# Optimization experiments

Hardware: AMD Instinct MI355X
Metric: run time of the kernel (lower is better)

## Reference

```python
import math
import jax, jax.numpy as jnp
import numpy as np

ETA = 0.3      # eta_threshold
EPS = 1e-08

B, S, C_IN, D_MODEL = 16, 2048, 64, 512


def setup_inputs() -> dict:
    key = jax.random.key(0)
    k1, k2, k3, k4 = jax.random.split(key, 4)
    x = jax.random.normal(k1, (B, S, C_IN), dtype=jnp.float32)
    # Conv1d(c_in, d_model, kernel=3, bias=False), kaiming fan_in
    fan_in = C_IN * 3
    conv_w = jax.random.normal(k2, (D_MODEL, C_IN, 3), dtype=jnp.float32) * (2.0 / fan_in) ** 0.5
    # Linear(1, d_model)
    tc_w = jax.random.normal(k3, (D_MODEL, 1), dtype=jnp.float32) * 0.5
    tc_b = jax.random.normal(k4, (D_MODEL,), dtype=jnp.float32) * 0.1
    return {"x": x, "conv_w": conv_w, "tc_w": tc_w, "tc_b": tc_b}


def compute_tc_vector(x):
    # x: (B, S, N_s). L1 norm over channels (beta_norm == 1).
    norms = jnp.sum(jnp.abs(x), axis=-1)            # (B, S)
    thresh = (1.0 - ETA) * (norms + EPS)            # condition: norms[s] < thresh[t]
    s = norms.shape[1]
    idx = jnp.arange(s)
    causal = idx[None, :] < idx[:, None]            # (T, S): s < t
    lt = norms[:, None, :] < thresh[:, :, None]     # (B, T, S)
    mask = lt & causal[None]
    # smallest tau = largest s with condition true; tau = t - s
    s_max = jnp.max(jnp.where(mask, idx[None, None, :], -1), axis=-1)  # (B, T)
    tc = jnp.where(s_max >= 0, idx[None, :] - s_max, 0)
    return tc.astype(jnp.float32)


def positional_embedding(seq_len, d_model):
    position = jnp.arange(seq_len, dtype=jnp.float32)[:, None]
    div_term = jnp.exp(jnp.arange(0, d_model, 2, dtype=jnp.float32) * (-math.log(10000.0) / d_model))
    ang = position * div_term                        # (S, D/2)
    pe = jnp.zeros((seq_len, d_model), dtype=jnp.float32)
    pe = pe.at[:, 0::2].set(jnp.sin(ang)).at[:, 1::2].set(jnp.cos(ang))
    return pe


def reference(x, conv_w, tc_w, tc_b):
    b, s, c = x.shape
    d = conv_w.shape[0]
    # Tc embedding: (B,S) -> Linear(1, D)
    tc = compute_tc_vector(x)                        # (B, S)
    tc_embed = tc[..., None] * tc_w[:, 0][None, None, :] + tc_b  # (B, S, D)
    # Token embedding: circular conv1d, k=3, pad 1 each side, no bias
    xc = jnp.transpose(x, (0, 2, 1))                 # (B, C, S)
    xp = jnp.concatenate([xc[..., -1:], xc, xc[..., :1]], axis=-1)
    conv = jax.lax.conv_general_dilated(xp, conv_w, window_strides=(1,), padding='VALID', dimension_numbers=('NCH', 'OIH', 'NCH'))
    val = jnp.transpose(conv, (0, 2, 1))             # (B, S, D)
    pe = positional_embedding(s, d)                  # (S, D)
    # dropout is identity in eval mode
    return val + pe[None] + tc_embed
```

## Files before the change

### kernel.cpp

```cpp
#include <hip/hip_runtime.h>
#include <hip/hip_bf16.h>

typedef __attribute__((ext_vector_type(8))) short bfrag;
typedef __attribute__((ext_vector_type(4))) float f32x4;

typedef __attribute__((address_space(1))) const void GV;
typedef __attribute__((address_space(3))) void LV;

static __device__ __forceinline__ float b2f(short s) {
    unsigned u = ((unsigned)(unsigned short)s) << 16;
    float f;
    __builtin_memcpy(&f, &u, 4);
    return f;
}

__global__ void k_prep(const float* __restrict__ x,
                       const float* __restrict__ w,
                       const float* __restrict__ tcb,
                       float* __restrict__ norms,
                       __hip_bfloat16* __restrict__ xb,
                       __hip_bfloat16* __restrict__ wt,
                       __hip_bfloat16* __restrict__ pe2b) {
    int blk = blockIdx.x;
    if (blk < 2048) {
        int i = blk * 256 + threadIdx.x;
        f32x4 v = *(const f32x4*)&x[i * 4];
        __hip_bfloat16 h[4];
        h[0] = __float2bfloat16(v.x);
        h[1] = __float2bfloat16(v.y);
        h[2] = __float2bfloat16(v.z);
        h[3] = __float2bfloat16(v.w);
        *(short4*)&xb[i * 4] = *(const short4*)h;
        float a = fabsf(v.x) + fabsf(v.y) + fabsf(v.z) + fabsf(v.w);
        a += __shfl_xor(a, 1);
        a += __shfl_xor(a, 2);
        a += __shfl_xor(a, 4);
        a += __shfl_xor(a, 8);
        if ((threadIdx.x & 15) == 0) norms[i >> 4] = a;
    } else if (blk < 2432) {
        int i = (blk - 2048) * 256 + threadIdx.x;
        int d = i / 192, kk = i - d * 192;
        int c = kk & 63, k = kk >> 6;
        wt[i] = __float2bfloat16(w[d * 192 + c * 3 + k]);
    } else {
        int j = (blk - 2432) * 256 + threadIdx.x;
        int s = j >> 7, q = j & 127;
        f32x4 tb = *(const f32x4*)&tcb[q * 4];
        float dv0 = expf((float)(4 * q)     * (-9.210340371976184f / 512.0f));
        float dv1 = expf((float)(4 * q + 2) * (-9.210340371976184f / 512.0f));
        float s0v, c0v, s1v, c1v;
        sincosf((float)s * dv0, &s0v, &c0v);
        sincosf((float)s * dv1, &s1v, &c1v);
        __hip_bfloat16 h[4];
        h[0] = __float2bfloat16(s0v + tb.x);
        h[1] = __float2bfloat16(c0v + tb.y);
        h[2] = __float2bfloat16(s1v + tb.z);
        h[3] = __float2bfloat16(c1v + tb.w);
        *(short4*)&pe2b[s * 512 + q * 4] = *(const short4*)h;
    }
}

__global__ void k_tc(const float* __restrict__ norms, float* __restrict__ tc) {
    int gid = blockIdx.x * 256 + threadIdx.x;
    int wave = gid >> 6;
    int lane = threadIdx.x & 63;
    int b = wave >> 11, t = wave & 2047;
    const float* nb = norms + (b << 11);
    float thresh = 0.7f * (nb[t] + 1e-8f);
    int res = 0;
    for (int W = (t - 1) >> 8; W >= 0; --W) {
        int sBase = W * 256 + 4 * lane;
        f32x4 v = *(const f32x4*)&nb[sBase];
        int best = -1;
        if (sBase + 0 < t && v.x < thresh) best = sBase + 0;
        if (sBase + 1 < t && v.y < thresh) best = sBase + 1;
        if (sBase + 2 < t && v.z < thresh) best = sBase + 2;
        if (sBase + 3 < t && v.w < thresh) best = sBase + 3;
        unsigned long long m = __ballot(best >= 0);
        if (m) {
            int L = 63 - __clzll(m);
            int smax = __shfl(best, L);
            res = t - smax;
            break;
        }
    }
    if (lane == 0) tc[wave] = (float)res;
}

__launch_bounds__(256, 3)
__global__ void k_gemm(const __hip_bfloat16* __restrict__ xb,
                       const __hip_bfloat16* __restrict__ wt,
                       const __hip_bfloat16* __restrict__ pe2b,
                       const float* __restrict__ tc,
                       const float* __restrict__ tcw,
                       float* __restrict__ out) {
    __shared__ alignas(16) __hip_bfloat16 Bs[130 * 64];
    __shared__ alignas(16) __hip_bfloat16 Ps[128 * 128];
    __shared__ alignas(16) float Ts[128];

    const int bid = blockIdx.x;
    const int xcd = bid & 7, u = bid >> 3;
    const int st = (xcd << 1) | (u & 1);
    const int bb = (u >> 1) & 15;
    const int d0 = (u >> 5) << 7;
    const int s0 = st << 7;
    const int tid = threadIdx.x;
    const int lane = tid & 63;
    const int wd = tid >> 6;
    const int lhi = lane >> 4, ll = lane & 15;

#pragma unroll
    for (int i = 0; i < 5; ++i) {
        int q = tid + i * 256;
        if (q < 1040) {
            int row = q >> 3, uu = q & 7;
            int us = uu ^ (row & 7);
            int sg = (s0 - 1 + row) & 2047;
            const __hip_bfloat16* src =
                xb + (size_t)((bb << 11) + sg) * 64 + us * 8;
            __builtin_amdgcn_global_load_lds((GV*)src, (LV*)(Bs + q * 8), 16, 0, 0);
        }
    }

    const __hip_bfloat16* wbase =
        wt + (size_t)(d0 + wd * 32 + ll) * 192 + lhi * 8;
    bfrag af[3][2][2];
#pragma unroll
    for (int k = 0; k < 3; ++k)
#pragma unroll
        for (int kc = 0; kc < 2; ++kc)
#pragma unroll
            for (int m = 0; m < 2; ++m)
                af[k][kc][m] = *(const bfrag*)(wbase + m * 16 * 192 +
                                               k * 64 + kc * 32);

    __syncthreads();

#pragma unroll
    for (int i = 0; i < 8; ++i) {
        int q = tid + i * 256;
        int sl = q >> 4, c = q & 15;
        int cs = c ^ (sl & 7);
        const __hip_bfloat16* src = pe2b + (size_t)(s0 + sl) * 512 + d0 + cs * 8;
        __builtin_amdgcn_global_load_lds((GV*)src, (LV*)(Ps + q * 8), 16, 0, 0);
    }
    if (tid < 32) {
        const float* src = tc + (bb << 11) + s0 + tid * 4;
        __builtin_amdgcn_global_load_lds((GV*)src, (LV*)(Ts + tid * 4), 16, 0, 0);
    }
    f32x4 tw[2];
#pragma unroll
    for (int m = 0; m < 2; ++m)
        tw[m] = *(const f32x4*)&tcw[d0 + wd * 32 + m * 16 + lhi * 4];

    f32x4 acc[2][8] = {};
#pragma unroll
    for (int k = 0; k < 3; ++k) {
#pragma unroll
        for (int kc = 0; kc < 2; ++kc) {
            const int colB = kc * 64 + lhi * 16;
            bfrag bf[8];
#pragma unroll
            for (int n = 0; n < 8; ++n) {
                int rl = n * 16 + ll + k;
                bf[n] = *(const bfrag*)((const char*)Bs + rl * 128 +
                                        (colB ^ ((rl & 7) << 4)));
            }
#pragma unroll
            for (int m = 0; m < 2; ++m)
#pragma unroll
                for (int n = 0; n < 8; ++n)
                    acc[m][n] = __builtin_amdgcn_mfma_f32_16x16x32_bf16(
                        af[k][kc][m], bf[n], acc[m][n], 0, 0, 0);
        }
    }

    __syncthreads();

#pragma unroll
    for (int n = 0; n < 8; ++n) {
        const int sl = n * 16 + ll;
        const int sCol = s0 + sl;
        const float tcv = Ts[sl];
        const size_t orow = ((size_t)(bb << 11) + sCol) * 512;
#pragma unroll
        for (int m = 0; m < 2; ++m) {
            const int dloc = wd * 32 + m * 16 + lhi * 4;
            const int pbyte = sl * 256 + ((((dloc >> 3) ^ (sl & 7)) << 4) |
                                          ((dloc << 1) & 15));
            const short4 pv = *(const short4*)((const char*)Ps + pbyte);
            f32x4 r = acc[m][n];
            r.x += b2f(pv.x) + tcv * tw[m].x;
            r.y += b2f(pv.y) + tcv * tw[m].y;
            r.z += b2f(pv.z) + tcv * tw[m].z;
            r.w += b2f(pv.w) + tcv * tw[m].w;
            *(f32x4*)&out[orow + d0 + dloc] = r;
        }
    }
}

extern "C" void kernel_launch(void* const* d_in, const int* in_sizes, int n_in,
                              void* d_out, int out_size, void* d_ws, size_t ws_size,
                              hipStream_t stream) {
    const float* x   = (const float*)d_in[0];
    const float* cw  = (const float*)d_in[1];
    const float* tcw = (const float*)d_in[2];
    const float* tcb = (const float*)d_in[3];
    float* out = (float*)d_out;

    char* ws = (char*)d_ws;
    __hip_bfloat16* xb   = (__hip_bfloat16*)(ws);
    __hip_bfloat16* wt   = (__hip_bfloat16*)(ws + 4194304);
    __hip_bfloat16* pe2b = (__hip_bfloat16*)(ws + 4390912);
    float* norms         = (float*)(ws + 6488064);
    float* tc            = (float*)(ws + 6619136);

    hipLaunchKernelGGL(k_prep, dim3(3456), dim3(256), 0, stream,
                       x, cw, tcb, norms, xb, wt, pe2b);
    hipLaunchKernelGGL(k_tc,   dim3(8192), dim3(256), 0, stream, norms, tc);
    hipLaunchKernelGGL(k_gemm, dim3(1024), dim3(256), 0, stream,
                       xb, wt, pe2b, tc, tcw, out);
}
```

Baseline: 40.25 us.

## Split positional tile into halves aliasing LDS to raise gemm occupancy

Cuts the gemm kernel's LDS footprint by loading the positional/bias tile in two 64-row halves. The second half reuses the input tile's LDS region once the MFMA loop has finished with it. Launch bounds go from 3 to 4 blocks per CU so more blocks can be resident. The cost is an extra barrier and loading the second half after compute, which exposes its latency in the epilogue. The tighter bound may also cause register spills.

```diff
diff --git a/kernel.cpp b/kernel.cpp
--- a/kernel.cpp
+++ b/kernel.cpp
@@ -87,16 +87,18 @@
     if (lane == 0) tc[wave] = (float)res;
 }
 
-__launch_bounds__(256, 3)
+__launch_bounds__(256, 4)
 __global__ void k_gemm(const __hip_bfloat16* __restrict__ xb,
                        const __hip_bfloat16* __restrict__ wt,
                        const __hip_bfloat16* __restrict__ pe2b,
                        const float* __restrict__ tc,
                        const float* __restrict__ tcw,
                        float* __restrict__ out) {
-    __shared__ alignas(16) __hip_bfloat16 Bs[130 * 64];
-    __shared__ alignas(16) __hip_bfloat16 Ps[128 * 128];
-    __shared__ alignas(16) float Ts[128];
+    __shared__ alignas(16) char Smem[33536];
+    __hip_bfloat16* Bs = (__hip_bfloat16*)Smem;
+    float* Ts          = (float*)(Smem + 16640);
+    char* Ps1          = Smem + 17152;
+    char* Ps2          = Smem;
 
     const int bid = blockIdx.x;
     const int xcd = bid & 7, u = bid >> 3;
@@ -121,6 +123,10 @@
             __builtin_amdgcn_global_load_lds((GV*)src, (LV*)(Bs + q * 8), 16, 0, 0);
         }
     }
+    if (tid < 32) {
+        const float* src = tc + (bb << 11) + s0 + tid * 4;
+        __builtin_amdgcn_global_load_lds((GV*)src, (LV*)(Ts + tid * 4), 16, 0, 0);
+    }
 
     const __hip_bfloat16* wbase =
         wt + (size_t)(d0 + wd * 32 + ll) * 192 + lhi * 8;
@@ -133,25 +139,21 @@
             for (int m = 0; m < 2; ++m)
                 af[k][kc][m] = *(const bfrag*)(wbase + m * 16 * 192 +
                                                k * 64 + kc * 32);
+    f32x4 tw[2];
+#pragma unroll
+    for (int m = 0; m < 2; ++m)
+        tw[m] = *(const f32x4*)&tcw[d0 + wd * 32 + m * 16 + lhi * 4];
 
     __syncthreads();
 
 #pragma unroll
-    for (int i = 0; i < 8; ++i) {
+    for (int i = 0; i < 4; ++i) {
         int q = tid + i * 256;
         int sl = q >> 4, c = q & 15;
         int cs = c ^ (sl & 7);
         const __hip_bfloat16* src = pe2b + (size_t)(s0 + sl) * 512 + d0 + cs * 8;
-        __builtin_amdgcn_global_load_lds((GV*)src, (LV*)(Ps + q * 8), 16, 0, 0);
-    }
-    if (tid < 32) {
-        const float* src = tc + (bb << 11) + s0 + tid * 4;
-        __builtin_amdgcn_global_load_lds((GV*)src, (LV*)(Ts + tid * 4), 16, 0, 0);
-    }
-    f32x4 tw[2];
-#pragma unroll
-    for (int m = 0; m < 2; ++m)
-        tw[m] = *(const f32x4*)&tcw[d0 + wd * 32 + m * 16 + lhi * 4];
+        __builtin_amdgcn_global_load_lds((GV*)src, (LV*)(Ps1 + q * 16), 16, 0, 0);
+    }
 
     f32x4 acc[2][8] = {};
 #pragma unroll
@@ -178,7 +180,17 @@
     __syncthreads();
 
 #pragma unroll
-    for (int n = 0; n < 8; ++n) {
+    for (int i = 0; i < 4; ++i) {
+        int q = tid + i * 256;
+        int r = q >> 4, c = q & 15;
+        int cs = c ^ (r & 7);
+        const __hip_bfloat16* src =
+            pe2b + (size_t)(s0 + 64 + r) * 512 + d0 + cs * 8;
+        __builtin_amdgcn_global_load_lds((GV*)src, (LV*)(Ps2 + q * 16), 16, 0, 0);
+    }
+
+#pragma unroll
+    for (int n = 0; n < 4; ++n) {
         const int sl = n * 16 + ll;
         const int sCol = s0 + sl;
         const float tcv = Ts[sl];
@@ -188,7 +200,31 @@
             const int dloc = wd * 32 + m * 16 + lhi * 4;
             const int pbyte = sl * 256 + ((((dloc >> 3) ^ (sl & 7)) << 4) |
                                           ((dloc << 1) & 15));
-            const short4 pv = *(const short4*)((const char*)Ps + pbyte);
+            const short4 pv = *(const short4*)(Ps1 + pbyte);
+            f32x4 r = acc[m][n];
+            r.x += b2f(pv.x) + tcv * tw[m].x;
+            r.y += b2f(pv.y) + tcv * tw[m].y;
+            r.z += b2f(pv.z) + tcv * tw[m].z;
+            r.w += b2f(pv.w) + tcv * tw[m].w;
+            *(f32x4*)&out[orow + d0 + dloc] = r;
+        }
+    }
+
+    __syncthreads();
+
+#pragma unroll
+    for (int n = 4; n < 8; ++n) {
+        const int sl = n * 16 + ll;
+        const int r2 = sl - 64;
+        const int sCol = s0 + sl;
+        const float tcv = Ts[sl];
+        const size_t orow = ((size_t)(bb << 11) + sCol) * 512;
+#pragma unroll
+        for (int m = 0; m < 2; ++m) {
+            const int dloc = wd * 32 + m * 16 + lhi * 4;
+            const int pbyte = r2 * 256 + ((((dloc >> 3) ^ (r2 & 7)) << 4) |
+                                          ((dloc << 1) & 15));
+            const short4 pv = *(const short4*)(Ps2 + pbyte);
             f32x4 r = acc[m][n];
             r.x += b2f(pv.x) + tcv * tw[m].x;
             r.y += b2f(pv.y) + tcv * tw[m].y;
```

Result: slower. 52.61 us (+30.7%).

## Process four batches per GEMM block to reuse weights and positional tile

Applied to the files above, without the earlier changes.

Each GEMM block now covers four batch elements for the same sequence/d_model tile. It loads all four x tiles into a larger shared buffer, and loads the weight fragments, PE tile and tc weights once, then loops over the batches. The grid shrinks from 1024 to 256 blocks and occupancy drops to one block per CU because of about 100KB of LDS. The aim is to cut redundant weight and PE loads, at the cost of less parallelism and latency hiding for a store-bound kernel.

```diff
diff --git a/kernel.cpp b/kernel.cpp
--- a/kernel.cpp
+++ b/kernel.cpp
@@ -87,22 +87,22 @@
     if (lane == 0) tc[wave] = (float)res;
 }
 
-__launch_bounds__(256, 3)
+__launch_bounds__(256, 1)
 __global__ void k_gemm(const __hip_bfloat16* __restrict__ xb,
                        const __hip_bfloat16* __restrict__ wt,
                        const __hip_bfloat16* __restrict__ pe2b,
                        const float* __restrict__ tc,
                        const float* __restrict__ tcw,
                        float* __restrict__ out) {
-    __shared__ alignas(16) __hip_bfloat16 Bs[130 * 64];
-    __shared__ alignas(16) __hip_bfloat16 Ps[128 * 128];
-    __shared__ alignas(16) float Ts[128];
+    __shared__ alignas(16) char Smem[101376];
+    char* Ps1 = Smem + 66560;
+    float* Ts = (float*)(Smem + 99328);
 
     const int bid = blockIdx.x;
-    const int xcd = bid & 7, u = bid >> 3;
-    const int st = (xcd << 1) | (u & 1);
-    const int bb = (u >> 1) & 15;
-    const int d0 = (u >> 5) << 7;
+    const int xcd = bid & 7, v = bid >> 3;
+    const int st = (xcd << 1) | (v & 1);
+    const int bbg = (v >> 1) & 3;
+    const int d0 = (v >> 3) << 7;
     const int s0 = st << 7;
     const int tid = threadIdx.x;
     const int lane = tid & 63;
@@ -110,91 +110,99 @@
     const int lhi = lane >> 4, ll = lane & 15;
 
 #pragma unroll
-    for (int i = 0; i < 5; ++i) {
-        int q = tid + i * 256;
-        if (q < 1040) {
-            int row = q >> 3, uu = q & 7;
-            int us = uu ^ (row & 7);
-            int sg = (s0 - 1 + row) & 2047;
-            const __hip_bfloat16* src =
-                xb + (size_t)((bb << 11) + sg) * 64 + us * 8;
-            __builtin_amdgcn_global_load_lds((GV*)src, (LV*)(Bs + q * 8), 16, 0, 0);
-        }
-    }
-
-    const __hip_bfloat16* wbase =
-        wt + (size_t)(d0 + wd * 32 + ll) * 192 + lhi * 8;
-    bfrag af[3][2][2];
-#pragma unroll
-    for (int k = 0; k < 3; ++k)
-#pragma unroll
-        for (int kc = 0; kc < 2; ++kc)
-#pragma unroll
-            for (int m = 0; m < 2; ++m)
-                af[k][kc][m] = *(const bfrag*)(wbase + m * 16 * 192 +
-                                               k * 64 + kc * 32);
-
-    __syncthreads();
-
+    for (int bi = 0; bi < 4; ++bi) {
+        const size_t xrow = (size_t)((bbg * 4 + bi) << 11);
+        char* Bsb = Smem + bi * 16640;
+#pragma unroll
+        for (int i = 0; i < 5; ++i) {
+            int q = tid + i * 256;
+            if (q < 1040) {
+                int row = q >> 3, uu = q & 7;
+                int us = uu ^ (row & 7);
+                int sg = (s0 - 1 + row) & 2047;
+                const __hip_bfloat16* src = xb + (xrow + sg) * 64 + us * 8;
+                __builtin_amdgcn_global_load_lds((GV*)src, (LV*)(Bsb + q * 16),
+                                                 16, 0, 0);
+            }
+        }
+    }
 #pragma unroll
     for (int i = 0; i < 8; ++i) {
         int q = tid + i * 256;
         int sl = q >> 4, c = q & 15;
         int cs = c ^ (sl & 7);
         const __hip_bfloat16* src = pe2b + (size_t)(s0 + sl) * 512 + d0 + cs * 8;
-        __builtin_amdgcn_global_load_lds((GV*)src, (LV*)(Ps + q * 8), 16, 0, 0);
-    }
-    if (tid < 32) {
-        const float* src = tc + (bb << 11) + s0 + tid * 4;
-        __builtin_amdgcn_global_load_lds((GV*)src, (LV*)(Ts + tid * 4), 16, 0, 0);
-    }
+        __builtin_amdgcn_global_load_lds((GV*)src, (LV*)(Ps1 + q * 16), 16, 0, 0);
+    }
+    if (tid < 128) {
+        int bi = tid >> 5, o = tid & 31;
+        const float* src = tc + ((size_t)((bbg * 4 + bi) << 11)) + s0 + o * 4;
+        __builtin_amdgcn_global_load_lds((GV*)src,
+                                         (LV*)(Ts + bi * 128 + o * 4), 16, 0, 0);
+    }
+
+    const __hip_bfloat16* wbase =
+        wt + (size_t)(d0 + wd * 32 + ll) * 192 + lhi * 8;
+    bfrag af[3][2][2];
+#pragma unroll
+    for (int k = 0; k < 3; ++k)
+#pragma unroll
+        for (int kc = 0; kc < 2; ++kc)
+#pragma unroll
+            for (int m = 0; m < 2; ++m)
+                af[k][kc][m] = *(const bfrag*)(wbase + m * 16 * 192 +
+                                               k * 64 + kc * 32);
     f32x4 tw[2];
 #pragma unroll
     for (int m = 0; m < 2; ++m)
         tw[m] = *(const f32x4*)&tcw[d0 + wd * 32 + m * 16 + lhi * 4];
 
-    f32x4 acc[2][8] = {};
-#pragma unroll
-    for (int k = 0; k < 3; ++k) {
-#pragma unroll
-        for (int kc = 0; kc < 2; ++kc) {
-            const int colB = kc * 64 + lhi * 16;
-            bfrag bf[8];
-#pragma unroll
-            for (int n = 0; n < 8; ++n) {
-                int rl = n * 16 + ll + k;
-                bf[n] = *(const bfrag*)((const char*)Bs + rl * 128 +
-                                        (colB ^ ((rl & 7) << 4)));
+    __syncthreads();
+
+#pragma unroll
+    for (int bi = 0; bi < 4; ++bi) {
+        const char* Bsb = Smem + bi * 16640;
+        f32x4 acc[2][8] = {};
+#pragma unroll
+        for (int k = 0; k < 3; ++k) {
+#pragma unroll
+            for (int kc = 0; kc < 2; ++kc) {
+                const int colB = kc * 64 + lhi * 16;
+                bfrag bf[8];
+#pragma unroll
+                for (int n = 0; n < 8; ++n) {
+                    int rl = n * 16 + ll + k;
+                    bf[n] = *(const bfrag*)(Bsb + rl * 128 +
+                                            (colB ^ ((rl & 7) << 4)));
+                }
+#pragma unroll
+                for (int m = 0; m < 2; ++m)
+#pragma unroll
+                    for (int n = 0; n < 8; ++n)
+                        acc[m][n] = __builtin_amdgcn_mfma_f32_16x16x32_bf16(
+                            af[k][kc][m], bf[n], acc[m][n], 0, 0, 0);
             }
-#pragma unroll
-            for (int m = 0; m < 2; ++m)
-#pragma unroll
-                for (int n = 0; n < 8; ++n)
-                    acc[m][n] = __builtin_amdgcn_mfma_f32_16x16x32_bf16(
-                        af[k][kc][m], bf[n], acc[m][n], 0, 0, 0);
-        }
-    }
-
-    __syncthreads();
-
-#pragma unroll
-    for (int n = 0; n < 8; ++n) {
-        const int sl = n * 16 + ll;
-        const int sCol = s0 + sl;
-        const float tcv = Ts[sl];
-        const size_t orow = ((size_t)(bb << 11) + sCol) * 512;
-#pragma unroll
-        for (int m = 0; m < 2; ++m) {
-            const int dloc = wd * 32 + m * 16 + lhi * 4;
-            const int pbyte = sl * 256 + ((((dloc >> 3) ^ (sl & 7)) << 4) |
-                                          ((dloc << 1) & 15));
-            const short4 pv = *(const short4*)((const char*)Ps + pbyte);
-            f32x4 r = acc[m][n];
-            r.x += b2f(pv.x) + tcv * tw[m].x;
-            r.y += b2f(pv.y) + tcv * tw[m].y;
-            r.z += b2f(pv.z) + tcv * tw[m].z;
-            r.w += b2f(pv.w) + tcv * tw[m].w;
-            *(f32x4*)&out[orow + d0 + dloc] = r;
+        }
+
+        const size_t obase = ((size_t)((bbg * 4 + bi) << 11) + s0) * 512;
+#pragma unroll
+        for (int n = 0; n < 8; ++n) {
+            const int sl = n * 16 + ll;
+            const float tcv = Ts[bi * 128 + sl];
+            const size_t orow = obase + (size_t)sl * 512;
+#pragma unroll
+            for (int m = 0; m < 2; ++m) {
+                const int dloc = wd * 32 + m * 16 + lhi * 4;
+                const int pbyte = sl * 256 + ((((dloc >> 3) ^ (sl & 7)) << 4) |
+                                              ((dloc << 1) & 15));
+                const short4 pv = *(const short4*)(Ps1 + pbyte);
+                f32x4 r = acc[m][n];
+                r.x += b2f(pv.x) + tcv * tw[m].x;
+                r.y += b2f(pv.y) + tcv * tw[m].y;
+                r.z += b2f(pv.z) + tcv * tw[m].z;
+                r.w += b2f(pv.w) + tcv * tw[m].w;
+                *(f32x4*)&out[orow + d0 + dloc] = r;
+            }
         }
     }
 }
@@ -218,6 +226,6 @@
     hipLaunchKernelGGL(k_prep, dim3(3456), dim3(256), 0, stream,
                        x, cw, tcb, norms, xb, wt, pe2b);
     hipLaunchKernelGGL(k_tc,   dim3(8192), dim3(256), 0, stream, norms, tc);
-    hipLaunchKernelGGL(k_gemm, dim3(1024), dim3(256), 0, stream,
+    hipLaunchKernelGGL(k_gemm, dim3(256),  dim3(256), 0, stream,
                        xb, wt, pe2b, tc, tcw, out);
 }
```

After: 37.12 us. -7.8%, faster.
